# Kernel optimization log

Hardware: AMD Instinct MI355X
Metric: run time of the kernel (lower is better)

Reference implementation:

```python
import jax, jax.numpy as jnp
import numpy as np

V, D, H, NL = 30000, 512, 8, 6
DH = D // H
B, L = 4, 1024
EPS = 1e-5


def setup_inputs() -> dict:
    key = jax.random.key(0)
    ks = jax.random.split(key, 16)
    s = 0.02
    n = lambda k, shape: jax.random.normal(k, shape, jnp.float32) * s
    return {
        'ids': jax.random.randint(ks[0], (B, L), 0, V),
        'embed': n(ks[1], (V, D)),
        'pos_enc': jax.random.normal(ks[2], (1, 1024, D), jnp.float32),
        'rg_w': n(ks[3], (NL, 4, D)), 'rg_b': jnp.zeros((NL, 4), jnp.float32),
        'qkv_w': n(ks[4], (NL, 3 * D, D)), 'qkv_b': jnp.zeros((NL, 3 * D), jnp.float32),
        'out_w': n(ks[5], (NL, D, D)), 'out_b': jnp.zeros((NL, D), jnp.float32),
        'phase_w': n(ks[6], (NL, H, D)), 'phase_b': jnp.zeros((NL, H), jnp.float32),
        'ff1_w': n(ks[7], (NL, 4 * D, D)), 'ff1_b': jnp.zeros((NL, 4 * D), jnp.float32),
        'ff2_w': n(ks[8], (NL, D, 4 * D)), 'ff2_b': jnp.zeros((NL, D), jnp.float32),
        'n1_s': jnp.ones((NL, D), jnp.float32), 'n1_b': jnp.zeros((NL, D), jnp.float32),
        'n2_s': jnp.ones((NL, D), jnp.float32), 'n2_b': jnp.zeros((NL, D), jnp.float32),
        'bnd_w1': n(ks[9], (D, D)), 'bnd_b1': jnp.zeros((D,), jnp.float32),
        'bnd_w2': n(ks[10], (1, D)), 'bnd_b2': jnp.zeros((1,), jnp.float32),
        'head_w': n(ks[11], (V, D)),
    }


def _ln(x, s, b):
    m = x.mean(-1, keepdims=True)
    v = ((x - m) ** 2).mean(-1, keepdims=True)
    return (x - m) * jax.lax.rsqrt(v + EPS) * s + b


def _block(x, p):
    rgw, rgb, qw, qb, ow, ob, pw, pb, f1w, f1b, f2w, f2b, s1, b1, s2, b2 = p
    Bc, Lc, _ = x.shape
    rg = jax.nn.sigmoid(x @ rgw.T + rgb)                       # [B,L,4]
    xm = x * (1.0 + rg.mean(-1, keepdims=True))
    h = _ln(xm, s1, b1)                                        # norm1(x_modulated)
    qkv = (h @ qw.T + qb).reshape(Bc, Lc, 3, H, DH)
    q, k, v = [jnp.transpose(qkv[:, :, i], (0, 2, 1, 3)) for i in range(3)]  # [B,H,L,dh]
    attn = jnp.einsum('bhid,bhjd->bhij', q, k) / (float(DH) ** 0.5)
    phase = jnp.transpose(h @ pw.T + pb, (0, 2, 1))            # [B,H,L]
    bias = -(phase[..., :, None] - phase[..., None, :]) ** 2   # [B,H,L,L]
    attn = jax.nn.softmax(attn + bias, axis=-1)
    ao = jnp.einsum('bhij,bhjd->bhid', attn, v)
    ao = jnp.transpose(ao, (0, 2, 1, 3)).reshape(Bc, Lc, D) @ ow.T + ob
    x = _ln(x + ao, s1, b1)
    ff = jax.nn.gelu(x @ f1w.T + f1b, approximate=False) @ f2w.T + f2b
    x = _ln(x + ff, s2, b2)
    return x, rg


def reference(ids, embed, pos_enc, rg_w, rg_b, qkv_w, qkv_b, out_w, out_b,
              phase_w, phase_b, ff1_w, ff1_b, ff2_w, ff2_b,
              n1_s, n1_b, n2_s, n2_b, bnd_w1, bnd_b1, bnd_w2, bnd_b2, head_w):
    Lc = ids.shape[1]
    x = embed[ids] + pos_enc[:, :Lc, :]
    layer_params = (rg_w, rg_b, qkv_w, qkv_b, out_w, out_b, phase_w, phase_b,
                    ff1_w, ff1_b, ff2_w, ff2_b, n1_s, n1_b, n2_s, n2_b)
    x, rgs = jax.lax.scan(_block, x, layer_params)
    gate = jax.nn.sigmoid((jnp.tanh(x @ bnd_w1.T + bnd_b1) @ bnd_w2.T + bnd_b2)[..., 0])
    logits = (x * gate[..., None]) @ head_w.T
    return logits, gate, rgs[-1]
```

## Files before the change

### kernel.cpp

```cpp
#include <hip/hip_runtime.h>
#include <math.h>

#define D 512
#define NH 8
#define DH 64
#define NL 6
#define Bsz 4
#define Lseq 1024
#define BL 4096
#define Vocab 30000
#define EPS 1e-5f

typedef __attribute__((ext_vector_type(8))) short s8v;
typedef __attribute__((ext_vector_type(4))) float f32x4;

__device__ __forceinline__ float sigmoidf_(float x) { return 1.0f / (1.0f + expf(-x)); }

__device__ __forceinline__ short f2bf(float f) {
  union { float f; unsigned u; } v; v.f = f;
  return (short)((v.u + 0x7FFFu + ((v.u >> 16) & 1u)) >> 16);
}
__device__ __forceinline__ float bf2f(short s) {
  union { unsigned u; float f; } v; v.u = ((unsigned)(unsigned short)s) << 16;
  return v.f;
}

__device__ __forceinline__ void gload16(const void* g, void* l) {
  __builtin_amdgcn_global_load_lds(
      (const __attribute__((address_space(1))) void*)g,
      (__attribute__((address_space(3))) void*)l, 16, 0, 0);
}

__global__ void f2bf_kernel(const float* __restrict__ in, short* __restrict__ out, int n) {
  int i = (blockIdx.x * 256 + threadIdx.x) * 8;
  if (i >= n) return;
  float4 a = *(const float4*)(in + i);
  float4 b = *(const float4*)(in + i + 4);
  s8v o;
  o[0] = f2bf(a.x); o[1] = f2bf(a.y); o[2] = f2bf(a.z); o[3] = f2bf(a.w);
  o[4] = f2bf(b.x); o[5] = f2bf(b.y); o[6] = f2bf(b.z); o[7] = f2bf(b.w);
  *(s8v*)(out + i) = o;
}

__global__ void embed_kernel(const int* __restrict__ ids, const float* __restrict__ emb,
                             const float* __restrict__ pos, float* __restrict__ x) {
  int tok = blockIdx.x;
  int l = tok & (Lseq - 1);
  int id = ids[tok];
  const float4* e = (const float4*)(emb + (size_t)id * D);
  const float4* p = (const float4*)(pos + (size_t)l * D);
  float4* o = (float4*)(x + (size_t)tok * D);
  float4 a = e[threadIdx.x], b = p[threadIdx.x];
  o[threadIdx.x] = make_float4(a.x + b.x, a.y + b.y, a.z + b.z, a.w + b.w);
}

__global__ __launch_bounds__(256) void rg_ln_kernel(
    const float* __restrict__ x, const float* __restrict__ rgw, const float* __restrict__ rgb,
    const float* __restrict__ sc, const float* __restrict__ bi,
    short* __restrict__ h, float* __restrict__ rg_out) {
  __shared__ float smg[4][4];
  __shared__ float sms[4][2];
  int tok = blockIdx.x, t = threadIdx.x, wid = t >> 6, lane = t & 63;
  const float* xr = x + (size_t)tok * D;
  float x0 = xr[t], x1 = xr[t + 256];
  float p0 = x0 * rgw[t]        + x1 * rgw[t + 256];
  float p1 = x0 * rgw[512 + t]  + x1 * rgw[512 + t + 256];
  float p2 = x0 * rgw[1024 + t] + x1 * rgw[1024 + t + 256];
  float p3 = x0 * rgw[1536 + t] + x1 * rgw[1536 + t + 256];
#pragma unroll
  for (int off = 32; off > 0; off >>= 1) {
    p0 += __shfl_xor(p0, off, 64);
    p1 += __shfl_xor(p1, off, 64);
    p2 += __shfl_xor(p2, off, 64);
    p3 += __shfl_xor(p3, off, 64);
  }
  if (lane == 0) { smg[wid][0] = p0; smg[wid][1] = p1; smg[wid][2] = p2; smg[wid][3] = p3; }
  __syncthreads();
  float g0 = sigmoidf_(smg[0][0] + smg[1][0] + smg[2][0] + smg[3][0] + rgb[0]);
  float g1 = sigmoidf_(smg[0][1] + smg[1][1] + smg[2][1] + smg[3][1] + rgb[1]);
  float g2 = sigmoidf_(smg[0][2] + smg[1][2] + smg[2][2] + smg[3][2] + rgb[2]);
  float g3 = sigmoidf_(smg[0][3] + smg[1][3] + smg[2][3] + smg[3][3] + rgb[3]);
  if (rg_out != nullptr && t == 0) {
    float* ro = rg_out + (size_t)tok * 4;
    ro[0] = g0; ro[1] = g1; ro[2] = g2; ro[3] = g3;
  }
  float mod = 1.0f + 0.25f * (g0 + g1 + g2 + g3);
  float m0 = x0 * mod, m1 = x1 * mod;
  float s = m0 + m1, q = m0 * m0 + m1 * m1;
#pragma unroll
  for (int off = 32; off > 0; off >>= 1) {
    s += __shfl_xor(s, off, 64);
    q += __shfl_xor(q, off, 64);
  }
  if (lane == 0) { sms[wid][0] = s; sms[wid][1] = q; }
  __syncthreads();
  float S = sms[0][0] + sms[1][0] + sms[2][0] + sms[3][0];
  float Q = sms[0][1] + sms[1][1] + sms[2][1] + sms[3][1];
  float mean = S * (1.0f / D);
  float var = Q * (1.0f / D) - mean * mean;
  float rstd = rsqrtf(var + EPS);
  h[(size_t)tok * D + t] = f2bf((m0 - mean) * rstd * sc[t] + bi[t]);
  h[(size_t)tok * D + t + 256] = f2bf((m1 - mean) * rstd * sc[t + 256] + bi[t + 256]);
}

__global__ __launch_bounds__(256) void residual_ln_kernel(
    float* __restrict__ x, const float* __restrict__ y,
    const float* __restrict__ sc, const float* __restrict__ bi,
    short* __restrict__ xb) {
  __shared__ float sms[4][2];
  int tok = blockIdx.x, t = threadIdx.x, wid = t >> 6, lane = t & 63;
  float v0 = x[(size_t)tok * D + t] + y[(size_t)tok * D + t];
  float v1 = x[(size_t)tok * D + t + 256] + y[(size_t)tok * D + t + 256];
  float s = v0 + v1, q = v0 * v0 + v1 * v1;
#pragma unroll
  for (int off = 32; off > 0; off >>= 1) {
    s += __shfl_xor(s, off, 64);
    q += __shfl_xor(q, off, 64);
  }
  if (lane == 0) { sms[wid][0] = s; sms[wid][1] = q; }
  __syncthreads();
  float S = sms[0][0] + sms[1][0] + sms[2][0] + sms[3][0];
  float Q = sms[0][1] + sms[1][1] + sms[2][1] + sms[3][1];
  float mean = S * (1.0f / D);
  float var = Q * (1.0f / D) - mean * mean;
  float rstd = rsqrtf(var + EPS);
  float o0 = (v0 - mean) * rstd * sc[t] + bi[t];
  float o1 = (v1 - mean) * rstd * sc[t + 256] + bi[t + 256];
  x[(size_t)tok * D + t] = o0;
  x[(size_t)tok * D + t + 256] = o1;
  xb[(size_t)tok * D + t] = f2bf(o0);
  xb[(size_t)tok * D + t + 256] = f2bf(o1);
}

template <bool OUTBF, bool NT>
__global__ __launch_bounds__(256) void gemm128_kernel(
    const short* __restrict__ A, const short* __restrict__ W,
    const float* __restrict__ bias, float* __restrict__ C, short* __restrict__ Cb,
    int M, int N, int K, int act) {
  __shared__ short As[128][32];
  __shared__ short Ws[128][32];
  int tid = threadIdx.x;
  int bn = blockIdx.x * 128, bm = blockIdx.y * 128;
  int wid = tid >> 6, lane = tid & 63;
  int wm = (wid >> 1) * 64, wn = (wid & 1) * 64;
  int fr = lane & 15, kg = lane >> 4;
  f32x4 acc[4][4] = {};
  int srow = 32 * wid + (lane >> 2);
  int scol = (lane & 3) * 8;
  const short* Ag0 = A + (size_t)(bm + srow) * K + scol;
  const short* Ag1 = Ag0 + (size_t)16 * K;
  int wr0 = bn + srow;       if (wr0 >= N) wr0 = N - 1;
  int wr1 = bn + srow + 16;  if (wr1 >= N) wr1 = N - 1;
  const short* Wg0 = W + (size_t)wr0 * K + scol;
  const short* Wg1 = W + (size_t)wr1 * K + scol;
  short* Al0 = &As[32 * wid][0];
  short* Al1 = &As[32 * wid + 16][0];
  short* Wl0 = &Ws[32 * wid][0];
  short* Wl1 = &Ws[32 * wid + 16][0];
  for (int k0 = 0; k0 < K; k0 += 32) {
    __syncthreads();
    gload16(Ag0 + k0, Al0);
    gload16(Ag1 + k0, Al1);
    gload16(Wg0 + k0, Wl0);
    gload16(Wg1 + k0, Wl1);
    __syncthreads();
    s8v af[4], bfv[4];
#pragma unroll
    for (int m = 0; m < 4; m++) af[m] = *(const s8v*)&As[wm + m * 16 + fr][kg * 8];
#pragma unroll
    for (int n = 0; n < 4; n++) bfv[n] = *(const s8v*)&Ws[wn + n * 16 + fr][kg * 8];
#pragma unroll
    for (int m = 0; m < 4; m++)
#pragma unroll
      for (int n = 0; n < 4; n++)
        acc[m][n] = __builtin_amdgcn_mfma_f32_16x16x32_bf16(af[m], bfv[n], acc[m][n], 0, 0, 0);
  }
  int rbase = bm + wm + kg * 4;
#pragma unroll
  for (int n = 0; n < 4; n++) {
    int col = bn + wn + n * 16 + fr;
    if (col >= N) continue;
    float bv = bias ? bias[col] : 0.0f;
#pragma unroll
    for (int m = 0; m < 4; m++) {
#pragma unroll
      for (int r = 0; r < 4; r++) {
        int row = rbase + m * 16 + r;
        float v = acc[m][n][r] + bv;
        if (act == 1) v = 0.5f * v * (1.0f + erff(v * 0.7071067811865475f));
        else if (act == 2) v = tanhf(v);
        if (OUTBF) Cb[(size_t)row * N + col] = f2bf(v);
        else if (NT) __builtin_nontemporal_store(v, &C[(size_t)row * N + col]);
        else C[(size_t)row * N + col] = v;
      }
    }
  }
}

template <bool OUTBF>
__global__ __launch_bounds__(256) void gemm64_kernel(
    const short* __restrict__ A, const short* __restrict__ W,
    const float* __restrict__ bias, float* __restrict__ C, short* __restrict__ Cb,
    short* __restrict__ Vt, int M, int N, int K, int act) {
  __shared__ short As[64][32];
  __shared__ short Ws[128][32];
  int tid = threadIdx.x;
  int bn = blockIdx.x * 128, bm = blockIdx.y * 64;
  int wid = tid >> 6, lane = tid & 63;
  int fr = lane & 15, kg = lane >> 4;
  f32x4 acc[4][2] = {};
  int l4 = lane >> 2;
  int scol = (lane & 3) * 8;
  const short* Ag0 = A + (size_t)(bm + 16 * wid + l4) * K + scol;
  int wr0 = bn + 32 * wid + l4;       if (wr0 >= N) wr0 = N - 1;
  int wr1 = bn + 32 * wid + 16 + l4;  if (wr1 >= N) wr1 = N - 1;
  const short* Wg0 = W + (size_t)wr0 * K + scol;
  const short* Wg1 = W + (size_t)wr1 * K + scol;
  short* Al0 = &As[16 * wid][0];
  short* Wl0 = &Ws[32 * wid][0];
  short* Wl1 = &Ws[32 * wid + 16][0];
  for (int k0 = 0; k0 < K; k0 += 32) {
    __syncthreads();
    gload16(Ag0 + k0, Al0);
    gload16(Wg0 + k0, Wl0);
    gload16(Wg1 + k0, Wl1);
    __syncthreads();
    s8v af[4], bfv[2];
#pragma unroll
    for (int m = 0; m < 4; m++) af[m] = *(const s8v*)&As[m * 16 + fr][kg * 8];
#pragma unroll
    for (int n = 0; n < 2; n++) bfv[n] = *(const s8v*)&Ws[wid * 32 + n * 16 + fr][kg * 8];
#pragma unroll
    for (int m = 0; m < 4; m++)
#pragma unroll
      for (int n = 0; n < 2; n++)
        acc[m][n] = __builtin_amdgcn_mfma_f32_16x16x32_bf16(af[m], bfv[n], acc[m][n], 0, 0, 0);
  }
  int rbase = bm + kg * 4;
#pragma unroll
  for (int n = 0; n < 2; n++) {
    int col = bn + wid * 32 + n * 16 + fr;
    if (col >= N) continue;
    float bv = bias ? bias[col] : 0.0f;
    if (Vt != nullptr && col >= 1024) {
      int hh = (col - 1024) >> 6, dd = (col - 1024) & 63;
#pragma unroll
      for (int m = 0; m < 4; m++) {
        int row0 = rbase + m * 16;
        int bb = row0 >> 10, ll = row0 & 1023;
        short4 pk;
        pk.x = f2bf(acc[m][n][0] + bv);
        pk.y = f2bf(acc[m][n][1] + bv);
        pk.z = f2bf(acc[m][n][2] + bv);
        pk.w = f2bf(acc[m][n][3] + bv);
        *(short4*)&Vt[((((size_t)bb * NH + hh) * DH + dd) << 10) | ll] = pk;
      }
      continue;
    }
#pragma unroll
    for (int m = 0; m < 4; m++) {
#pragma unroll
      for (int r = 0; r < 4; r++) {
        int row = rbase + m * 16 + r;
        float v = acc[m][n][r] + bv;
        if (act == 1) v = 0.5f * v * (1.0f + erff(v * 0.7071067811865475f));
        else if (act == 2) v = tanhf(v);
        if (OUTBF) Cb[(size_t)row * N + col] = f2bf(v);
        else C[(size_t)row * N + col] = v;
      }
    }
  }
}

template <bool OUTBF>
__global__ __launch_bounds__(256) void gemm_conv_kernel(
    const short* __restrict__ A, const float* __restrict__ Wp,
    const float* __restrict__ bias, float* __restrict__ C, short* __restrict__ Cb,
    short* __restrict__ Vt, int M, int N, int K, int act) {
  __shared__ short As[128][40];
  __shared__ short Ws[128][40];
  int tid = threadIdx.x;
  int bn = blockIdx.x * 128, bm = blockIdx.y * 128;
  int wid = tid >> 6, lane = tid & 63;
  int wm = (wid >> 1) * 64, wn = (wid & 1) * 64;
  int fr = lane & 15, kg = lane >> 4;
  f32x4 acc[4][4] = {};
  int sr = tid >> 1;
  int sc = (tid & 1) * 16;
  const short* Arow = A + (size_t)(bm + sr) * K + sc;
  int wrow = bn + sr;
  int wclamp = wrow < N ? wrow : 0;
  const float* Wrow_f = Wp + (size_t)wclamp * K + sc;
  for (int k0 = 0; k0 < K; k0 += 32) {
    s8v a0 = *(const s8v*)(Arow + k0);
    s8v a1 = *(const s8v*)(Arow + k0 + 8);
    s8v w0, w1;
    float4 f0 = *(const float4*)(Wrow_f + k0);
    float4 f1 = *(const float4*)(Wrow_f + k0 + 4);
    float4 f2 = *(const float4*)(Wrow_f + k0 + 8);
    float4 f3 = *(const float4*)(Wrow_f + k0 + 12);
    w0[0] = f2bf(f0.x); w0[1] = f2bf(f0.y); w0[2] = f2bf(f0.z); w0[3] = f2bf(f0.w);
    w0[4] = f2bf(f1.x); w0[5] = f2bf(f1.y); w0[6] = f2bf(f1.z); w0[7] = f2bf(f1.w);
    w1[0] = f2bf(f2.x); w1[1] = f2bf(f2.y); w1[2] = f2bf(f2.z); w1[3] = f2bf(f2.w);
    w1[4] = f2bf(f3.x); w1[5] = f2bf(f3.y); w1[6] = f2bf(f3.z); w1[7] = f2bf(f3.w);
    __syncthreads();
    *(s8v*)&As[sr][sc] = a0;
    *(s8v*)&As[sr][sc + 8] = a1;
    *(s8v*)&Ws[sr][sc] = w0;
    *(s8v*)&Ws[sr][sc + 8] = w1;
    __syncthreads();
    s8v af[4], bfv[4];
#pragma unroll
    for (int m = 0; m < 4; m++) af[m] = *(const s8v*)&As[wm + m * 16 + fr][kg * 8];
#pragma unroll
    for (int n = 0; n < 4; n++) bfv[n] = *(const s8v*)&Ws[wn + n * 16 + fr][kg * 8];
#pragma unroll
    for (int m = 0; m < 4; m++)
#pragma unroll
      for (int n = 0; n < 4; n++)
        acc[m][n] = __builtin_amdgcn_mfma_f32_16x16x32_bf16(af[m], bfv[n], acc[m][n], 0, 0, 0);
  }
  int rbase = bm + wm + kg * 4;
#pragma unroll
  for (int n = 0; n < 4; n++) {
    int col = bn + wn + n * 16 + fr;
    if (col >= N) continue;
    float bv = bias ? bias[col] : 0.0f;
    if (Vt != nullptr && col >= 1024) {
      int hh = (col - 1024) >> 6, dd = (col - 1024) & 63;
#pragma unroll
      for (int m = 0; m < 4; m++) {
        int row0 = rbase + m * 16;
        int bb = row0 >> 10, ll = row0 & 1023;
        short4 pk;
        pk.x = f2bf(acc[m][n][0] + bv);
        pk.y = f2bf(acc[m][n][1] + bv);
        pk.z = f2bf(acc[m][n][2] + bv);
        pk.w = f2bf(acc[m][n][3] + bv);
        *(short4*)&Vt[((((size_t)bb * NH + hh) * DH + dd) << 10) | ll] = pk;
      }
      continue;
    }
#pragma unroll
    for (int m = 0; m < 4; m++) {
#pragma unroll
      for (int r = 0; r < 4; r++) {
        int row = rbase + m * 16 + r;
        float v = acc[m][n][r] + bv;
        if (act == 1) v = 0.5f * v * (1.0f + erff(v * 0.7071067811865475f));
        else if (act == 2) v = tanhf(v);
        if (OUTBF) Cb[(size_t)row * N + col] = f2bf(v);
        else C[(size_t)row * N + col] = v;
      }
    }
  }
}

__global__ __launch_bounds__(256) void phase_kernel(
    const short* __restrict__ hbf, const float* __restrict__ pw,
    const float* __restrict__ pb, float* __restrict__ phase) {
  int tok = blockIdx.x, t = threadIdx.x;
  int h = t >> 5, ln = t & 31;
  const short* hr = hbf + (size_t)tok * D;
  const s8v* hv = (const s8v*)(hr + ln * 16);
  s8v h0 = hv[0], h1 = hv[1];
  const float4* wv = (const float4*)(pw + (size_t)h * D + ln * 16);
  float4 w0 = wv[0], w1 = wv[1], w2 = wv[2], w3 = wv[3];
  float acc = 0.f;
  acc += bf2f(h0[0]) * w0.x + bf2f(h0[1]) * w0.y + bf2f(h0[2]) * w0.z + bf2f(h0[3]) * w0.w;
  acc += bf2f(h0[4]) * w1.x + bf2f(h0[5]) * w1.y + bf2f(h0[6]) * w1.z + bf2f(h0[7]) * w1.w;
  acc += bf2f(h1[0]) * w2.x + bf2f(h1[1]) * w2.y + bf2f(h1[2]) * w2.z + bf2f(h1[3]) * w2.w;
  acc += bf2f(h1[4]) * w3.x + bf2f(h1[5]) * w3.y + bf2f(h1[6]) * w3.z + bf2f(h1[7]) * w3.w;
  for (int off = 16; off > 0; off >>= 1) acc += __shfl_down(acc, off, 32);
  if (ln == 0) phase[(size_t)tok * NH + h] = acc + pb[h];
}

__global__ __launch_bounds__(256) void mha_kernel(
    const short* __restrict__ qkv, const short* __restrict__ vt,
    const float* __restrict__ phase, short* __restrict__ out) {
  __shared__ short sQ[64][72];
  __shared__ short sK[64][72];
  __shared__ short sVt[64][72];
  __shared__ short sP[64][72];
  __shared__ float sPh[Lseq];
  int bh = blockIdx.y;
  int b = bh >> 3, h = bh & 7;
  int q0 = blockIdx.x * 64;
  int tid = threadIdx.x;
  int lane = tid & 63, wid = tid >> 6;
  int fr = lane & 15, kg = lane >> 4;
  int wm = wid * 16;
  const short* vtb = vt + ((size_t)bh * DH) * Lseq;

  for (int j = tid; j < Lseq; j += 256) sPh[j] = phase[((size_t)(b * Lseq + j)) * NH + h];
  for (int idx = tid; idx < 512; idx += 256) {
    int row = idx >> 3, c8 = (idx & 7) * 8;
    *(s8v*)&sQ[row][c8] =
        *(const s8v*)(qkv + (((size_t)(b * Lseq + q0 + row)) * 3 + 0) * D + h * DH + c8);
  }
  __syncthreads();

  float phq[4];
#pragma unroll
  for (int r = 0; r < 4; r++) phq[r] = sPh[q0 + wm + kg * 4 + r];

  float mrow[4] = {-1e30f, -1e30f, -1e30f, -1e30f};
  float lrow[4] = {0.f, 0.f, 0.f, 0.f};
  f32x4 o[4] = {};

  for (int kt = 0; kt < Lseq / 64; kt++) {
    int k0 = kt * 64;
    __syncthreads();
    for (int idx = tid; idx < 512; idx += 256) {
      int row = idx >> 3, c8 = (idx & 7) * 8;
      *(s8v*)&sK[row][c8] =
          *(const s8v*)(qkv + (((size_t)(b * Lseq + k0 + row)) * 3 + 1) * D + h * DH + c8);
      *(s8v*)&sVt[row][c8] = *(const s8v*)(vtb + (size_t)row * Lseq + k0 + c8);
    }
    __syncthreads();

    s8v qa0 = *(const s8v*)&sQ[wm + fr][kg * 8];
    s8v qa1 = *(const s8v*)&sQ[wm + fr][32 + kg * 8];
    f32x4 sacc[4];
#pragma unroll
    for (int n = 0; n < 4; n++) {
      f32x4 z = {};
      s8v kb0 = *(const s8v*)&sK[n * 16 + fr][kg * 8];
      s8v kb1 = *(const s8v*)&sK[n * 16 + fr][32 + kg * 8];
      z = __builtin_amdgcn_mfma_f32_16x16x32_bf16(qa0, kb0, z, 0, 0, 0);
      z = __builtin_amdgcn_mfma_f32_16x16x32_bf16(qa1, kb1, z, 0, 0, 0);
      sacc[n] = z;
    }
    float sv[4][4];
#pragma unroll
    for (int n = 0; n < 4; n++) {
      float phk = sPh[k0 + n * 16 + fr];
#pragma unroll
      for (int r = 0; r < 4; r++) {
        float dp = phq[r] - phk;
        sv[n][r] = sacc[n][r] * 0.125f - dp * dp;
      }
    }
    float mnew[4], alpha[4];
#pragma unroll
    for (int r = 0; r < 4; r++) {
      float mx = fmaxf(fmaxf(sv[0][r], sv[1][r]), fmaxf(sv[2][r], sv[3][r]));
#pragma unroll
      for (int off = 1; off < 16; off <<= 1) mx = fmaxf(mx, __shfl_xor(mx, off, 64));
      mnew[r] = fmaxf(mrow[r], mx);
      alpha[r] = __expf(mrow[r] - mnew[r]);
      mrow[r] = mnew[r];
    }
    float rs[4] = {0.f, 0.f, 0.f, 0.f};
#pragma unroll
    for (int n = 0; n < 4; n++) {
#pragma unroll
      for (int r = 0; r < 4; r++) {
        float p = __expf(sv[n][r] - mnew[r]);
        rs[r] += p;
        sP[wm + kg * 4 + r][n * 16 + fr] = f2bf(p);
      }
    }
#pragma unroll
    for (int r = 0; r < 4; r++) {
#pragma unroll
      for (int off = 1; off < 16; off <<= 1) rs[r] += __shfl_xor(rs[r], off, 64);
      lrow[r] = lrow[r] * alpha[r] + rs[r];
    }
#pragma unroll
    for (int df = 0; df < 4; df++) {
      o[df][0] *= alpha[0]; o[df][1] *= alpha[1];
      o[df][2] *= alpha[2]; o[df][3] *= alpha[3];
    }
    s8v pa0 = *(const s8v*)&sP[wm + fr][kg * 8];
    s8v pa1 = *(const s8v*)&sP[wm + fr][32 + kg * 8];
#pragma unroll
    for (int df = 0; df < 4; df++) {
      int d = df * 16 + fr;
      s8v vb0 = *(const s8v*)&sVt[d][kg * 8];
      s8v vb1 = *(const s8v*)&sVt[d][32 + kg * 8];
      o[df] = __builtin_amdgcn_mfma_f32_16x16x32_bf16(pa0, vb0, o[df], 0, 0, 0);
      o[df] = __builtin_amdgcn_mfma_f32_16x16x32_bf16(pa1, vb1, o[df], 0, 0, 0);
    }
  }
  float inv[4];
#pragma unroll
  for (int r = 0; r < 4; r++) inv[r] = 1.0f / lrow[r];
#pragma unroll
  for (int df = 0; df < 4; df++) {
#pragma unroll
    for (int r = 0; r < 4; r++) {
      int row = q0 + wm + kg * 4 + r;
      out[((size_t)(b * Lseq + row)) * D + h * DH + df * 16 + fr] = f2bf(o[df][r] * inv[r]);
    }
  }
}

__global__ void gate_kernel(const float* __restrict__ tb, const float* __restrict__ w2,
                            const float* __restrict__ b2, float* __restrict__ gate) {
  int tok = blockIdx.x;
  int lane = threadIdx.x;
  const float* row = tb + (size_t)tok * D;
  float acc = 0.f;
  for (int d = lane; d < D; d += 64) acc += row[d] * w2[d];
  for (int off = 32; off > 0; off >>= 1) acc += __shfl_down(acc, off, 64);
  if (lane == 0) gate[tok] = 1.0f / (1.0f + expf(-(acc + b2[0])));
}

__global__ void xg_kernel(const float* __restrict__ x, const float* __restrict__ gate,
                          short* __restrict__ xg) {
  int tok = blockIdx.x, t = threadIdx.x;
  float g = gate[tok];
  float4 v = *(const float4*)(x + (size_t)tok * D + t * 4);
  short4 o = make_short4(f2bf(v.x * g), f2bf(v.y * g), f2bf(v.z * g), f2bf(v.w * g));
  *(short4*)(xg + (size_t)tok * D + t * 4) = o;
}

extern "C" void kernel_launch(void* const* d_in, const int* in_sizes, int n_in,
                              void* d_out, int out_size, void* d_ws, size_t ws_size,
                              hipStream_t stream) {
  const int* ids = (const int*)d_in[0];
  const float* emb = (const float*)d_in[1];
  const float* pos = (const float*)d_in[2];
  const float* rg_w = (const float*)d_in[3];
  const float* rg_b = (const float*)d_in[4];
  const float* qkv_w = (const float*)d_in[5];
  const float* qkv_b = (const float*)d_in[6];
  const float* out_w = (const float*)d_in[7];
  const float* out_b = (const float*)d_in[8];
  const float* ph_w = (const float*)d_in[9];
  const float* ph_b = (const float*)d_in[10];
  const float* ff1_w = (const float*)d_in[11];
  const float* ff1_b = (const float*)d_in[12];
  const float* ff2_w = (const float*)d_in[13];
  const float* ff2_b = (const float*)d_in[14];
  const float* n1_s = (const float*)d_in[15];
  const float* n1_b = (const float*)d_in[16];
  const float* n2_s = (const float*)d_in[17];
  const float* n2_b = (const float*)d_in[18];
  const float* bw1 = (const float*)d_in[19];
  const float* bb1 = (const float*)d_in[20];
  const float* bw2 = (const float*)d_in[21];
  const float* bb2 = (const float*)d_in[22];
  const float* head_w = (const float*)d_in[23];

  char* w = (char*)d_ws;
  float* x      = (float*)(w + 0);
  float* ao     = (float*)(w + 8388608);
  float* phase  = (float*)(w + 16777216);
  short* h_bf   = (short*)(w + 16908288);
  short* ao_bf  = (short*)(w + 21102592);
  short* x_bf   = (short*)(w + 25296896);
  short* ff_bf  = (short*)(w + 29491200);
  short* xg_bf  = (short*)(w + 46268416);
  short* qkv_bf = (short*)(w + 50462720);
  short* vt_bf  = (short*)(w + 63045632);
  short* wqkv   = (short*)(w + 67239936);
  short* wout   = (short*)(w + 76677120);
  short* wff1   = (short*)(w + 79822848);
  short* wff2   = (short*)(w + 92405760);
  short* wbnd   = (short*)(w + 104988672);
  short* whead  = (short*)(w + 105512960);
  const size_t WS_FULL = 136232960;

  float* outf   = (float*)d_out;
  float* logits = outf;
  float* gate   = outf + 122880000;
  float* rg_out = outf + 122884096;

  bool fast = ws_size >= WS_FULL;

  if (fast) {
    f2bf_kernel<<<(4718592 / 8 + 255) / 256, 256, 0, stream>>>(qkv_w, wqkv, 4718592);
    f2bf_kernel<<<(1572864 / 8 + 255) / 256, 256, 0, stream>>>(out_w, wout, 1572864);
    f2bf_kernel<<<(6291456 / 8 + 255) / 256, 256, 0, stream>>>(ff1_w, wff1, 6291456);
    f2bf_kernel<<<(6291456 / 8 + 255) / 256, 256, 0, stream>>>(ff2_w, wff2, 6291456);
    f2bf_kernel<<<(262144 / 8 + 255) / 256, 256, 0, stream>>>(bw1, wbnd, 262144);
    f2bf_kernel<<<(15360000 / 8 + 255) / 256, 256, 0, stream>>>(head_w, whead, 15360000);
  }

  embed_kernel<<<BL, 128, 0, stream>>>(ids, emb, pos, x);

  for (int l = 0; l < NL; l++) {
    rg_ln_kernel<<<BL, 256, 0, stream>>>(
        x, rg_w + (size_t)l * 4 * D, rg_b + l * 4, n1_s + l * D, n1_b + l * D,
        h_bf, (l == NL - 1) ? rg_out : nullptr);
    if (fast)
      gemm64_kernel<true><<<dim3(12, 64), 256, 0, stream>>>(
          h_bf, wqkv + (size_t)l * 1536 * D, qkv_b + l * 1536, nullptr, qkv_bf, vt_bf,
          BL, 1536, D, 0);
    else
      gemm_conv_kernel<true><<<dim3(12, 32), 256, 0, stream>>>(
          h_bf, qkv_w + (size_t)l * 1536 * D, qkv_b + l * 1536, nullptr, qkv_bf, vt_bf,
          BL, 1536, D, 0);
    phase_kernel<<<BL, 256, 0, stream>>>(h_bf, ph_w + (size_t)l * NH * D, ph_b + l * NH, phase);
    mha_kernel<<<dim3(Lseq / 64, Bsz * NH), 256, 0, stream>>>(qkv_bf, vt_bf, phase, ao_bf);
    if (fast)
      gemm64_kernel<false><<<dim3(4, 64), 256, 0, stream>>>(
          ao_bf, wout + (size_t)l * D * D, out_b + l * D, ao, nullptr, nullptr, BL, D, D, 0);
    else
      gemm_conv_kernel<false><<<dim3(4, 32), 256, 0, stream>>>(
          ao_bf, out_w + (size_t)l * D * D, out_b + l * D, ao, nullptr, nullptr, BL, D, D, 0);
    residual_ln_kernel<<<BL, 256, 0, stream>>>(x, ao, n1_s + l * D, n1_b + l * D, x_bf);
    if (fast)
      gemm64_kernel<true><<<dim3(16, 64), 256, 0, stream>>>(
          x_bf, wff1 + (size_t)l * 2048 * D, ff1_b + l * 2048, nullptr, ff_bf, nullptr,
          BL, 2048, D, 1);
    else
      gemm_conv_kernel<true><<<dim3(16, 32), 256, 0, stream>>>(
          x_bf, ff1_w + (size_t)l * 2048 * D, ff1_b + l * 2048, nullptr, ff_bf, nullptr,
          BL, 2048, D, 1);
    if (fast)
      gemm64_kernel<false><<<dim3(4, 64), 256, 0, stream>>>(
          ff_bf, wff2 + (size_t)l * D * 2048, ff2_b + l * D, ao, nullptr, nullptr,
          BL, D, 2048, 0);
    else
      gemm_conv_kernel<false><<<dim3(4, 32), 256, 0, stream>>>(
          ff_bf, ff2_w + (size_t)l * D * 2048, ff2_b + l * D, ao, nullptr, nullptr,
          BL, D, 2048, 0);
    residual_ln_kernel<<<BL, 256, 0, stream>>>(x, ao, n2_s + l * D, n2_b + l * D, x_bf);
  }

  if (fast)
    gemm64_kernel<false><<<dim3(4, 64), 256, 0, stream>>>(
        x_bf, wbnd, bb1, ao, nullptr, nullptr, BL, D, D, 2);
  else
    gemm_conv_kernel<false><<<dim3(4, 32), 256, 0, stream>>>(
        x_bf, bw1, bb1, ao, nullptr, nullptr, BL, D, D, 2);
  gate_kernel<<<BL, 64, 0, stream>>>(ao, bw2, bb2, gate);
  xg_kernel<<<BL, 128, 0, stream>>>(x, gate, xg_bf);
  if (fast)
    gemm128_kernel<false, true><<<dim3(235, 32), 256, 0, stream>>>(
        xg_bf, whead, nullptr, logits, nullptr, BL, Vocab, D, 0);
  else
    gemm_conv_kernel<false><<<dim3(235, 32), 256, 0, stream>>>(
        xg_bf, head_w, nullptr, logits, nullptr, nullptr, BL, Vocab, D, 0);
}
```

Before: 1.322 ms.

## Double-buffer GEMM shared-memory tiles and store residual branch outputs as bf16

Both MFMA GEMM kernels now use two shared-memory buffers. The next K tile is loaded while the current one feeds the MFMAs, which leaves one barrier per iteration instead of two. Separately, the out-projection and FF2 GEMMs write bf16 instead of fp32, and the residual LayerNorm reads bf16, halving that intermediate traffic. The bf16 residual adds rounding error, and the doubled LDS per block may lower occupancy.

New measurement: 1.272 ms. 1.04x faster.

```diff
diff --git a/kernel.cpp b/kernel.cpp
--- a/kernel.cpp
+++ b/kernel.cpp
@@ -104,13 +104,13 @@
 }
 
 __global__ __launch_bounds__(256) void residual_ln_kernel(
-    float* __restrict__ x, const float* __restrict__ y,
+    float* __restrict__ x, const short* __restrict__ y,
     const float* __restrict__ sc, const float* __restrict__ bi,
     short* __restrict__ xb) {
   __shared__ float sms[4][2];
   int tok = blockIdx.x, t = threadIdx.x, wid = t >> 6, lane = t & 63;
-  float v0 = x[(size_t)tok * D + t] + y[(size_t)tok * D + t];
-  float v1 = x[(size_t)tok * D + t + 256] + y[(size_t)tok * D + t + 256];
+  float v0 = x[(size_t)tok * D + t] + bf2f(y[(size_t)tok * D + t]);
+  float v1 = x[(size_t)tok * D + t + 256] + bf2f(y[(size_t)tok * D + t + 256]);
   float s = v0 + v1, q = v0 * v0 + v1 * v1;
 #pragma unroll
   for (int off = 32; off > 0; off >>= 1) {
@@ -137,8 +137,8 @@
     const short* __restrict__ A, const short* __restrict__ W,
     const float* __restrict__ bias, float* __restrict__ C, short* __restrict__ Cb,
     int M, int N, int K, int act) {
-  __shared__ short As[128][32];
-  __shared__ short Ws[128][32];
+  __shared__ short As[2][128][32];
+  __shared__ short Ws[2][128][32];
   int tid = threadIdx.x;
   int bn = blockIdx.x * 128, bm = blockIdx.y * 128;
   int wid = tid >> 6, lane = tid & 63;
@@ -153,27 +153,33 @@
   int wr1 = bn + srow + 16;  if (wr1 >= N) wr1 = N - 1;
   const short* Wg0 = W + (size_t)wr0 * K + scol;
   const short* Wg1 = W + (size_t)wr1 * K + scol;
-  short* Al0 = &As[32 * wid][0];
-  short* Al1 = &As[32 * wid + 16][0];
-  short* Wl0 = &Ws[32 * wid][0];
-  short* Wl1 = &Ws[32 * wid + 16][0];
-  for (int k0 = 0; k0 < K; k0 += 32) {
-    __syncthreads();
-    gload16(Ag0 + k0, Al0);
-    gload16(Ag1 + k0, Al1);
-    gload16(Wg0 + k0, Wl0);
-    gload16(Wg1 + k0, Wl1);
-    __syncthreads();
+  short* AsF = &As[0][0][0];
+  short* WsF = &Ws[0][0][0];
+  auto stage = [&](int buf, int k0) {
+    gload16(Ag0 + k0, AsF + buf * 4096 + (32 * wid) * 32);
+    gload16(Ag1 + k0, AsF + buf * 4096 + (32 * wid + 16) * 32);
+    gload16(Wg0 + k0, WsF + buf * 4096 + (32 * wid) * 32);
+    gload16(Wg1 + k0, WsF + buf * 4096 + (32 * wid + 16) * 32);
+  };
+  stage(0, 0);
+  __syncthreads();
+  int nt = K / 32, cur = 0;
+  for (int t = 0; t < nt; ++t) {
+    if (t + 1 < nt) stage(cur ^ 1, (t + 1) * 32);
+    const short* ab = AsF + cur * 4096;
+    const short* wb = WsF + cur * 4096;
     s8v af[4], bfv[4];
 #pragma unroll
-    for (int m = 0; m < 4; m++) af[m] = *(const s8v*)&As[wm + m * 16 + fr][kg * 8];
-#pragma unroll
-    for (int n = 0; n < 4; n++) bfv[n] = *(const s8v*)&Ws[wn + n * 16 + fr][kg * 8];
+    for (int m = 0; m < 4; m++) af[m] = *(const s8v*)(ab + (wm + m * 16 + fr) * 32 + kg * 8);
+#pragma unroll
+    for (int n = 0; n < 4; n++) bfv[n] = *(const s8v*)(wb + (wn + n * 16 + fr) * 32 + kg * 8);
 #pragma unroll
     for (int m = 0; m < 4; m++)
 #pragma unroll
       for (int n = 0; n < 4; n++)
         acc[m][n] = __builtin_amdgcn_mfma_f32_16x16x32_bf16(af[m], bfv[n], acc[m][n], 0, 0, 0);
+    __syncthreads();
+    cur ^= 1;
   }
   int rbase = bm + wm + kg * 4;
 #pragma unroll
@@ -202,8 +208,8 @@
     const short* __restrict__ A, const short* __restrict__ W,
     const float* __restrict__ bias, float* __restrict__ C, short* __restrict__ Cb,
     short* __restrict__ Vt, int M, int N, int K, int act) {
-  __shared__ short As[64][32];
-  __shared__ short Ws[128][32];
+  __shared__ short As[2][64][32];
+  __shared__ short Ws[2][128][32];
   int tid = threadIdx.x;
   int bn = blockIdx.x * 128, bm = blockIdx.y * 64;
   int wid = tid >> 6, lane = tid & 63;
@@ -216,25 +222,32 @@
   int wr1 = bn + 32 * wid + 16 + l4;  if (wr1 >= N) wr1 = N - 1;
   const short* Wg0 = W + (size_t)wr0 * K + scol;
   const short* Wg1 = W + (size_t)wr1 * K + scol;
-  short* Al0 = &As[16 * wid][0];
-  short* Wl0 = &Ws[32 * wid][0];
-  short* Wl1 = &Ws[32 * wid + 16][0];
-  for (int k0 = 0; k0 < K; k0 += 32) {
-    __syncthreads();
-    gload16(Ag0 + k0, Al0);
-    gload16(Wg0 + k0, Wl0);
-    gload16(Wg1 + k0, Wl1);
-    __syncthreads();
+  short* AsF = &As[0][0][0];
+  short* WsF = &Ws[0][0][0];
+  auto stage = [&](int buf, int k0) {
+    gload16(Ag0 + k0, AsF + buf * 2048 + (16 * wid) * 32);
+    gload16(Wg0 + k0, WsF + buf * 4096 + (32 * wid) * 32);
+    gload16(Wg1 + k0, WsF + buf * 4096 + (32 * wid + 16) * 32);
+  };
+  stage(0, 0);
+  __syncthreads();
+  int nt = K / 32, cur = 0;
+  for (int t = 0; t < nt; ++t) {
+    if (t + 1 < nt) stage(cur ^ 1, (t + 1) * 32);
+    const short* ab = AsF + cur * 2048;
+    const short* wb = WsF + cur * 4096;
     s8v af[4], bfv[2];
 #pragma unroll
-    for (int m = 0; m < 4; m++) af[m] = *(const s8v*)&As[m * 16 + fr][kg * 8];
-#pragma unroll
-    for (int n = 0; n < 2; n++) bfv[n] = *(const s8v*)&Ws[wid * 32 + n * 16 + fr][kg * 8];
+    for (int m = 0; m < 4; m++) af[m] = *(const s8v*)(ab + (m * 16 + fr) * 32 + kg * 8);
+#pragma unroll
+    for (int n = 0; n < 2; n++) bfv[n] = *(const s8v*)(wb + (wid * 32 + n * 16 + fr) * 32 + kg * 8);
 #pragma unroll
     for (int m = 0; m < 4; m++)
 #pragma unroll
       for (int n = 0; n < 2; n++)
         acc[m][n] = __builtin_amdgcn_mfma_f32_16x16x32_bf16(af[m], bfv[n], acc[m][n], 0, 0, 0);
+    __syncthreads();
+    cur ^= 1;
   }
   int rbase = bm + kg * 4;
 #pragma unroll
@@ -547,6 +560,7 @@
   char* w = (char*)d_ws;
   float* x      = (float*)(w + 0);
   float* ao     = (float*)(w + 8388608);
+  short* y_bf   = (short*)(w + 8388608);
   float* phase  = (float*)(w + 16777216);
   short* h_bf   = (short*)(w + 16908288);
   short* ao_bf  = (short*)(w + 21102592);
@@ -596,12 +610,12 @@
     phase_kernel<<<BL, 256, 0, stream>>>(h_bf, ph_w + (size_t)l * NH * D, ph_b + l * NH, phase);
     mha_kernel<<<dim3(Lseq / 64, Bsz * NH), 256, 0, stream>>>(qkv_bf, vt_bf, phase, ao_bf);
     if (fast)
-      gemm64_kernel<false><<<dim3(4, 64), 256, 0, stream>>>(
-          ao_bf, wout + (size_t)l * D * D, out_b + l * D, ao, nullptr, nullptr, BL, D, D, 0);
+      gemm64_kernel<true><<<dim3(4, 64), 256, 0, stream>>>(
+          ao_bf, wout + (size_t)l * D * D, out_b + l * D, nullptr, y_bf, nullptr, BL, D, D, 0);
     else
-      gemm_conv_kernel<false><<<dim3(4, 32), 256, 0, stream>>>(
-          ao_bf, out_w + (size_t)l * D * D, out_b + l * D, ao, nullptr, nullptr, BL, D, D, 0);
-    residual_ln_kernel<<<BL, 256, 0, stream>>>(x, ao, n1_s + l * D, n1_b + l * D, x_bf);
+      gemm_conv_kernel<true><<<dim3(4, 32), 256, 0, stream>>>(
+          ao_bf, out_w + (size_t)l * D * D, out_b + l * D, nullptr, y_bf, nullptr, BL, D, D, 0);
+    residual_ln_kernel<<<BL, 256, 0, stream>>>(x, y_bf, n1_s + l * D, n1_b + l * D, x_bf);
     if (fast)
       gemm64_kernel<true><<<dim3(16, 64), 256, 0, stream>>>(
           x_bf, wff1 + (size_t)l * 2048 * D, ff1_b + l * 2048, nullptr, ff_bf, nullptr,
@@ -611,14 +625,14 @@
           x_bf, ff1_w + (size_t)l * 2048 * D, ff1_b + l * 2048, nullptr, ff_bf, nullptr,
           BL, 2048, D, 1);
     if (fast)
-      gemm64_kernel<false><<<dim3(4, 64), 256, 0, stream>>>(
-          ff_bf, wff2 + (size_t)l * D * 2048, ff2_b + l * D, ao, nullptr, nullptr,
+      gemm64_kernel<true><<<dim3(4, 64), 256, 0, stream>>>(
+          ff_bf, wff2 + (size_t)l * D * 2048, ff2_b + l * D, nullptr, y_bf, nullptr,
           BL, D, 2048, 0);
     else
-      gemm_conv_kernel<false><<<dim3(4, 32), 256, 0, stream>>>(
-          ff_bf, ff2_w + (size_t)l * D * 2048, ff2_b + l * D, ao, nullptr, nullptr,
+      gemm_conv_kernel<true><<<dim3(4, 32), 256, 0, stream>>>(
+          ff_bf, ff2_w + (size_t)l * D * 2048, ff2_b + l * D, nullptr, y_bf, nullptr,
           BL, D, 2048, 0);
-    residual_ln_kernel<<<BL, 256, 0, stream>>>(x, ao, n2_s + l * D, n2_b + l * D, x_bf);
+    residual_ln_kernel<<<BL, 256, 0, stream>>>(x, y_bf, n2_s + l * D, n2_b + l * D, x_bf);
   }
 
   if (fast)
```
